# Kernel tuning notes

Hardware: AMD Instinct MI355X
Metric: run time of the kernel (lower is better)

Reference implementation:

```python
import jax, jax.numpy as jnp
import numpy as np

HEADS = 12
DIM_HEAD = 64
SCALE = DIM_HEAD ** -0.5


def setup_inputs() -> dict:
    key = jax.random.key(0)
    k1, k2, k3 = jax.random.split(key, 3)
    B, N, D = 4, 2048, 768
    inner = HEADS * DIM_HEAD  # 768
    x = jax.random.normal(k1, (B, N, D), dtype=jnp.float32)
    W_qkv = jax.random.normal(k2, (D, 3 * inner), dtype=jnp.float32) * (D ** -0.5)
    W_out = jax.random.normal(k3, (inner, D), dtype=jnp.float32) * (inner ** -0.5)
    b_out = jnp.zeros((D,), dtype=jnp.float32)
    return {"x": x, "W_qkv": W_qkv, "W_out": W_out, "b_out": b_out}


def reference(x, W_qkv, W_out, b_out):
    B, N, D = x.shape
    qkv = x @ W_qkv  # [B, N, 3*inner]
    q, k, v = jnp.split(qkv, 3, axis=-1)
    # 'b n (h d) -> b h n d'
    def split_heads(t):
        return t.reshape(B, N, HEADS, DIM_HEAD).transpose(0, 2, 1, 3)
    q, k, v = split_heads(q), split_heads(k), split_heads(v)
    dots = jnp.einsum('bhnd,bhmd->bhnm', q, k) * SCALE  # [B, H, N, N]
    attn = jax.nn.softmax(dots, axis=-1)
    out = jnp.einsum('bhnm,bhmd->bhnd', attn, v)
    out = out.transpose(0, 2, 1, 3).reshape(B, N, HEADS * DIM_HEAD)  # 'b h n d -> b n (h d)'
    return out @ W_out + b_out
```

## Files before the change

### kernel.cpp

```cpp
#include <hip/hip_runtime.h>
#include <hip/hip_bf16.h>

typedef __bf16 bf16_t;
typedef __bf16 bf16x4 __attribute__((ext_vector_type(4)));
typedef __bf16 bf16x8 __attribute__((ext_vector_type(8)));
typedef float f32x4 __attribute__((ext_vector_type(4)));

#define HEADS 12
#define DHEAD 64
#define NSEQ 2048
#define BATCH 4
#define DMODEL 768
#define NINNER 768

__device__ __forceinline__ void gl_lds16(const bf16_t* g, bf16_t* l) {
  __builtin_amdgcn_global_load_lds(
      (const __attribute__((address_space(1))) void*)g,
      (__attribute__((address_space(3))) void*)l, 16, 0, 0);
}

__device__ __forceinline__ int swz(int row, int colElem) {
  return row * 64 + (colElem ^ ((row & 7) << 3));
}

__global__ void cast_bf16_kernel(const float* __restrict__ in, bf16_t* __restrict__ out, int n8) {
  int i = blockIdx.x * blockDim.x + threadIdx.x;
  const int stride = gridDim.x * blockDim.x;
  for (; i < n8; i += stride) {
    const f32x4* p = (const f32x4*)(in + (size_t)i * 8);
    f32x4 a = p[0], b = p[1];
    bf16x8 o;
#pragma unroll
    for (int j = 0; j < 4; ++j) { o[j] = (bf16_t)a[j]; o[j + 4] = (bf16_t)b[j]; }
    *(bf16x8*)(out + (size_t)i * 8) = o;
  }
}

__global__ void transpose_cast_kernel(const float* __restrict__ in, bf16_t* __restrict__ out,
                                      int K, int N) {
  __shared__ float tile[32][33];
  const int bx = blockIdx.x * 32;
  const int by = blockIdx.y * 32;
  const int tx = threadIdx.x, ty = threadIdx.y;
#pragma unroll
  for (int i = ty; i < 32; i += 8)
    tile[i][tx] = in[(size_t)(by + i) * N + bx + tx];
  __syncthreads();
#pragma unroll
  for (int i = ty; i < 32; i += 8)
    out[(size_t)(bx + i) * K + by + tx] = (bf16_t)tile[tx][i];
}

template <int MODE>
__global__ __launch_bounds__(256, 2)
void gemm_bt(const bf16_t* __restrict__ A, const bf16_t* __restrict__ Bt,
             bf16_t* __restrict__ qw, bf16_t* __restrict__ kw, bf16_t* __restrict__ vtw,
             const float* __restrict__ bias, float* __restrict__ outf,
             int M, int Nn, int K) {
  __shared__ bf16_t As[128 * 64];
  __shared__ bf16_t Bs[128 * 64];
  const int tid = threadIdx.x;
  const int wid = tid >> 6;
  const int lane = tid & 63;
  const int m0 = blockIdx.x * 128;
  const int n0 = blockIdx.y * 128;
  const int arow = lane >> 3;
  const int acol = (lane & 7) * 8;
  const int wm = (wid >> 1) * 64;
  const int wn = (wid & 1) * 64;
  const int fr = lane & 15;
  const int fg = lane >> 4;

  f32x4 acc[4][4] = {};

  for (int kt = 0; kt < K; kt += 64) {
    __syncthreads();
#pragma unroll
    for (int i = 0; i < 4; ++i) {
      const int c = i * 4 + wid;
      gl_lds16(A + (size_t)(m0 + c * 8 + arow) * K + kt + acol, As + c * 512);
      gl_lds16(Bt + (size_t)(n0 + c * 8 + arow) * K + kt + acol, Bs + c * 512);
    }
    __syncthreads();
#pragma unroll
    for (int kk = 0; kk < 2; ++kk) {
      bf16x8 af[4], bfr[4];
#pragma unroll
      for (int mi = 0; mi < 4; ++mi)
        af[mi] = *(const bf16x8*)(As + (wm + mi * 16 + fr) * 64 + kk * 32 + fg * 8);
#pragma unroll
      for (int ni = 0; ni < 4; ++ni)
        bfr[ni] = *(const bf16x8*)(Bs + (wn + ni * 16 + fr) * 64 + kk * 32 + fg * 8);
#pragma unroll
      for (int mi = 0; mi < 4; ++mi)
#pragma unroll
        for (int ni = 0; ni < 4; ++ni)
          acc[mi][ni] = __builtin_amdgcn_mfma_f32_16x16x32_bf16(af[mi], bfr[ni], acc[mi][ni], 0, 0, 0);
    }
  }

  if (MODE == 0 && n0 >= 2 * NINNER) {
#pragma unroll
    for (int mi = 0; mi < 4; ++mi) {
#pragma unroll
      for (int ni = 0; ni < 4; ++ni) {
        const int col = n0 + wn + ni * 16 + fr - 2 * NINNER;
        const int h = col >> 6, d = col & 63;
        const int row0 = m0 + wm + mi * 16 + fg * 4;
        const int b = row0 >> 11, n = row0 & 2047;
        bf16x4 pk;
#pragma unroll
        for (int r = 0; r < 4; ++r) pk[r] = (bf16_t)acc[mi][ni][r];
        *(bf16x4*)(vtw + ((size_t)((b * HEADS + h) * DHEAD + d)) * NSEQ + n) = pk;
      }
    }
  } else {
#pragma unroll
    for (int mi = 0; mi < 4; ++mi) {
#pragma unroll
      for (int ni = 0; ni < 4; ++ni) {
#pragma unroll
        for (int r = 0; r < 4; ++r) {
          const int row = m0 + wm + mi * 16 + fg * 4 + r;
          const int col = n0 + wn + ni * 16 + fr;
          float val = acc[mi][ni][r];
          if (MODE == 0) {
            const int which = col / NINNER;
            const int cin = col - which * NINNER;
            const int h = cin >> 6, d = cin & 63;
            const int b = row >> 11, n = row & 2047;
            bf16_t* dst = (which == 0) ? qw : kw;
            if (which == 0) val *= 0.125f;
            dst[(((size_t)(b * HEADS + h)) * NSEQ + n) * DHEAD + d] = (bf16_t)val;
          } else {
            outf[(size_t)row * Nn + col] = val + bias[col];
          }
        }
      }
    }
  }
}

__global__ __launch_bounds__(256, 3)
void attn_fwd(const bf16_t* __restrict__ qg, const bf16_t* __restrict__ kg,
              const bf16_t* __restrict__ vtg, bf16_t* __restrict__ og) {
  __shared__ bf16_t Ks[2][64 * 64];
  __shared__ bf16_t Vs[2][64 * 64];
  __shared__ bf16_t Ps[4 * 32 * 64];
  const int tid = threadIdx.x, wid = tid >> 6, lane = tid & 63;
  const int logical = (blockIdx.x & 7) * 96 + (blockIdx.x >> 3);
  const int bh = logical >> 4;
  const int qbase = (logical & 15) * 128 + wid * 32;
  const bf16_t* Q = qg + (size_t)bh * NSEQ * DHEAD;
  const bf16_t* K = kg + (size_t)bh * NSEQ * DHEAD;
  const bf16_t* Vt = vtg + (size_t)bh * NSEQ * DHEAD;
  const int fr = lane & 15, fg = lane >> 4;

  bf16x8 qf[2][2];
#pragma unroll
  for (int mi = 0; mi < 2; ++mi)
#pragma unroll
    for (int ks = 0; ks < 2; ++ks)
      qf[mi][ks] = *(const bf16x8*)(Q + (size_t)(qbase + mi * 16 + fr) * DHEAD + ks * 32 + fg * 8);

  f32x4 oacc[2][4] = {};
  float lsum[2][4] = {{0.f, 0.f, 0.f, 0.f}, {0.f, 0.f, 0.f, 0.f}};
  bf16_t* myP = Ps + wid * (32 * 64);

  const int krow = lane >> 3;
  const int ksrc = ((lane & 7) ^ krow) << 3;

#pragma unroll
  for (int i = 0; i < 2; ++i) {
    const int c = wid * 2 + i;
    gl_lds16(K + (size_t)(c * 8 + krow) * DHEAD + ksrc, &Ks[0][c * 512]);
    gl_lds16(Vt + (size_t)(c * 8 + krow) * NSEQ + ksrc, &Vs[0][c * 512]);
  }

  for (int t = 0; t < NSEQ / 64; ++t) {
    const int buf = t & 1;
    __syncthreads();

    if (t + 1 < NSEQ / 64) {
      const int kv = (t + 1) * 64;
#pragma unroll
      for (int i = 0; i < 2; ++i) {
        const int c = wid * 2 + i;
        gl_lds16(K + (size_t)(kv + c * 8 + krow) * DHEAD + ksrc, &Ks[buf ^ 1][c * 512]);
        gl_lds16(Vt + (size_t)(c * 8 + krow) * NSEQ + kv + ksrc, &Vs[buf ^ 1][c * 512]);
      }
    }

    f32x4 sacc[2][4] = {};
    __builtin_amdgcn_s_setprio(1);
#pragma unroll
    for (int ks = 0; ks < 2; ++ks) {
      bf16x8 kf[4];
#pragma unroll
      for (int ni = 0; ni < 4; ++ni)
        kf[ni] = *(const bf16x8*)(&Ks[buf][swz(ni * 16 + fr, ks * 32 + fg * 8)]);
#pragma unroll
      for (int mi = 0; mi < 2; ++mi)
#pragma unroll
        for (int ni = 0; ni < 4; ++ni)
          sacc[mi][ni] = __builtin_amdgcn_mfma_f32_16x16x32_bf16(qf[mi][ks], kf[ni], sacc[mi][ni], 0, 0, 0);
    }
    __builtin_amdgcn_s_setprio(0);

#pragma unroll
    for (int mi = 0; mi < 2; ++mi) {
#pragma unroll
      for (int r = 0; r < 4; ++r) {
        float rs = 0.f;
#pragma unroll
        for (int ni = 0; ni < 4; ++ni) {
          float p = __expf(sacc[mi][ni][r]);
          sacc[mi][ni][r] = p;
          rs += p;
        }
        lsum[mi][r] += rs;
      }
    }

#pragma unroll
    for (int mi = 0; mi < 2; ++mi)
#pragma unroll
      for (int ni = 0; ni < 4; ++ni)
#pragma unroll
        for (int r = 0; r < 4; ++r) {
          const int row = mi * 16 + fg * 4 + r;
          myP[row * 64 + ((ni * 16 + fr) ^ ((row & 7) << 3))] = (bf16_t)sacc[mi][ni][r];
        }
    asm volatile("s_waitcnt lgkmcnt(0)" ::: "memory");
    __builtin_amdgcn_sched_barrier(0);

    __builtin_amdgcn_s_setprio(1);
#pragma unroll
    for (int ks = 0; ks < 2; ++ks) {
      bf16x8 pf[2], vf[4];
#pragma unroll
      for (int mi = 0; mi < 2; ++mi)
        pf[mi] = *(const bf16x8*)(myP + swz(mi * 16 + fr, ks * 32 + fg * 8));
#pragma unroll
      for (int di = 0; di < 4; ++di)
        vf[di] = *(const bf16x8*)(&Vs[buf][swz(di * 16 + fr, ks * 32 + fg * 8)]);
#pragma unroll
      for (int mi = 0; mi < 2; ++mi)
#pragma unroll
        for (int di = 0; di < 4; ++di)
          oacc[mi][di] = __builtin_amdgcn_mfma_f32_16x16x32_bf16(pf[mi], vf[di], oacc[mi][di], 0, 0, 0);
    }
    __builtin_amdgcn_s_setprio(0);
  }

#pragma unroll
  for (int mi = 0; mi < 2; ++mi)
#pragma unroll
    for (int r = 0; r < 4; ++r) {
      float rs = lsum[mi][r];
#pragma unroll
      for (int mk = 8; mk >= 1; mk >>= 1) rs += __shfl_xor(rs, mk, 64);
      lsum[mi][r] = rs;
    }

  const int b = bh / HEADS, h = bh % HEADS;
#pragma unroll
  for (int mi = 0; mi < 2; ++mi) {
#pragma unroll
    for (int r = 0; r < 4; ++r) {
      const int n = qbase + mi * 16 + fg * 4 + r;
      const float inv = 1.0f / lsum[mi][r];
#pragma unroll
      for (int di = 0; di < 4; ++di)
        og[((size_t)b * NSEQ + n) * DMODEL + h * DHEAD + di * 16 + fr] =
            (bf16_t)(oacc[mi][di][r] * inv);
    }
  }
}

extern "C" void kernel_launch(void* const* d_in, const int* in_sizes, int n_in,
                              void* d_out, int out_size, void* d_ws, size_t ws_size,
                              hipStream_t stream) {
  const float* x    = (const float*)d_in[0];
  const float* Wqkv = (const float*)d_in[1];
  const float* Wout = (const float*)d_in[2];
  const float* bout = (const float*)d_in[3];
  float* out = (float*)d_out;

  char* ws = (char*)d_ws;
  bf16_t* xb    = (bf16_t*)(ws + 0);
  bf16_t* wqkvT = (bf16_t*)(ws + 12582912);
  bf16_t* woutT = (bf16_t*)(ws + 16121856);
  bf16_t* qw    = (bf16_t*)(ws + 17301504);
  bf16_t* kw    = (bf16_t*)(ws + 29884416);
  bf16_t* vtw   = (bf16_t*)(ws + 42467328);
  bf16_t* attno = (bf16_t*)(ws + 55050240);

  cast_bf16_kernel<<<1024, 256, 0, stream>>>(x, xb, (8192 * 768) / 8);
  transpose_cast_kernel<<<dim3(2304 / 32, 768 / 32), dim3(32, 8), 0, stream>>>(Wqkv, wqkvT, 768, 2304);
  transpose_cast_kernel<<<dim3(768 / 32, 768 / 32), dim3(32, 8), 0, stream>>>(Wout, woutT, 768, 768);

  gemm_bt<0><<<dim3(64, 18), 256, 0, stream>>>(xb, wqkvT, qw, kw, vtw, nullptr, nullptr,
                                               8192, 2304, 768);
  attn_fwd<<<768, 256, 0, stream>>>(qw, kw, vtw, attno);
  gemm_bt<1><<<dim3(64, 6), 256, 0, stream>>>(attno, woutT, nullptr, nullptr, nullptr, bout, out,
                                              8192, 768, 768);
}
```

Baseline: 159.2 us.

## Rewrite attention core with 32x32 MFMA and register-resident P via lane shuffles

Switches the attention kernel from 16x16x32 to 32x32x16 bf16 MFMA tiles and computes S transposed (K as the A operand), so P stays in registers. P is packed to bf16 and exchanged across half-waves with shuffles instead of going through an LDS round-trip. K/V staging becomes a single unswizzled buffer laid out in per-fragment order, and the row-sum reduction shrinks to one cross-half shuffle. This removes the P LDS stores and loads, the lgkmcnt wait and the swizzle arithmetic, but adds shuffle traffic and more accumulator registers, which puts the 3-wave occupancy target at risk.

```diff
diff --git a/kernel.cpp b/kernel.cpp
--- a/kernel.cpp
+++ b/kernel.cpp
@@ -5,6 +5,8 @@
 typedef __bf16 bf16x4 __attribute__((ext_vector_type(4)));
 typedef __bf16 bf16x8 __attribute__((ext_vector_type(8)));
 typedef float f32x4 __attribute__((ext_vector_type(4)));
+typedef float f32x16 __attribute__((ext_vector_type(16)));
+typedef unsigned int u32x4 __attribute__((ext_vector_type(4)));
 
 #define HEADS 12
 #define DHEAD 64
@@ -19,8 +21,10 @@
       (__attribute__((address_space(3))) void*)l, 16, 0, 0);
 }
 
-__device__ __forceinline__ int swz(int row, int colElem) {
-  return row * 64 + (colElem ^ ((row & 7) << 3));
+__device__ __forceinline__ unsigned pack_bf16_2(float a, float b) {
+  unsigned lo = (unsigned)__builtin_bit_cast(unsigned short, (bf16_t)a);
+  unsigned hi = (unsigned)__builtin_bit_cast(unsigned short, (bf16_t)b);
+  return lo | (hi << 16);
 }
 
 __global__ void cast_bf16_kernel(const float* __restrict__ in, bf16_t* __restrict__ out, int n8) {
@@ -144,9 +148,7 @@
 __global__ __launch_bounds__(256, 3)
 void attn_fwd(const bf16_t* __restrict__ qg, const bf16_t* __restrict__ kg,
               const bf16_t* __restrict__ vtg, bf16_t* __restrict__ og) {
-  __shared__ bf16_t Ks[2][64 * 64];
-  __shared__ bf16_t Vs[2][64 * 64];
-  __shared__ bf16_t Ps[4 * 32 * 64];
+  __shared__ bf16_t KV[2][16 * 512];
   const int tid = threadIdx.x, wid = tid >> 6, lane = tid & 63;
   const int logical = (blockIdx.x & 7) * 96 + (blockIdx.x >> 3);
   const int bh = logical >> 4;
@@ -154,127 +156,102 @@
   const bf16_t* Q = qg + (size_t)bh * NSEQ * DHEAD;
   const bf16_t* K = kg + (size_t)bh * NSEQ * DHEAD;
   const bf16_t* Vt = vtg + (size_t)bh * NSEQ * DHEAD;
-  const int fr = lane & 15, fg = lane >> 4;
-
-  bf16x8 qf[2][2];
-#pragma unroll
-  for (int mi = 0; mi < 2; ++mi)
-#pragma unroll
-    for (int ks = 0; ks < 2; ++ks)
-      qf[mi][ks] = *(const bf16x8*)(Q + (size_t)(qbase + mi * 16 + fr) * DHEAD + ks * 32 + fg * 8);
-
-  f32x4 oacc[2][4] = {};
-  float lsum[2][4] = {{0.f, 0.f, 0.f, 0.f}, {0.f, 0.f, 0.f, 0.f}};
-  bf16_t* myP = Ps + wid * (32 * 64);
-
-  const int krow = lane >> 3;
-  const int ksrc = ((lane & 7) ^ krow) << 3;
-
-#pragma unroll
-  for (int i = 0; i < 2; ++i) {
-    const int c = wid * 2 + i;
-    gl_lds16(K + (size_t)(c * 8 + krow) * DHEAD + ksrc, &Ks[0][c * 512]);
-    gl_lds16(Vt + (size_t)(c * 8 + krow) * NSEQ + ksrc, &Vs[0][c * 512]);
-  }
+  const int l31 = lane & 31, hi = lane >> 5;
+
+  bf16x8 qf[4];
+#pragma unroll
+  for (int ks = 0; ks < 4; ++ks)
+    qf[ks] = *(const bf16x8*)(Q + (size_t)(qbase + l31) * DHEAD + ks * 16 + hi * 8);
+
+  f32x16 oacc[2] = {};
+  float lsum = 0.f;
+
+  auto stage = [&](int bsel, int t) {
+    const int kv0 = t * 64;
+#pragma unroll
+    for (int i = 0; i < 4; ++i) {
+      const int c = wid * 4 + i;
+      bf16_t* dst = &KV[bsel][c * 512];
+      if (c < 8) {
+        gl_lds16(K + (size_t)(kv0 + (c >> 2) * 32 + l31) * DHEAD + (c & 3) * 16 + hi * 8, dst);
+      } else {
+        gl_lds16(Vt + (size_t)(((c >> 2) & 1) * 32 + l31) * NSEQ + kv0 + (c & 3) * 16 + hi * 8, dst);
+      }
+    }
+  };
+
+  stage(0, 0);
 
   for (int t = 0; t < NSEQ / 64; ++t) {
     const int buf = t & 1;
     __syncthreads();
-
-    if (t + 1 < NSEQ / 64) {
-      const int kv = (t + 1) * 64;
-#pragma unroll
-      for (int i = 0; i < 2; ++i) {
-        const int c = wid * 2 + i;
-        gl_lds16(K + (size_t)(kv + c * 8 + krow) * DHEAD + ksrc, &Ks[buf ^ 1][c * 512]);
-        gl_lds16(Vt + (size_t)(c * 8 + krow) * NSEQ + kv + ksrc, &Vs[buf ^ 1][c * 512]);
-      }
-    }
-
-    f32x4 sacc[2][4] = {};
+    if (t + 1 < NSEQ / 64) stage(buf ^ 1, t + 1);
+
+    const bf16_t* base = &KV[buf][0];
+
+    f32x16 sacc[2] = {};
     __builtin_amdgcn_s_setprio(1);
 #pragma unroll
-    for (int ks = 0; ks < 2; ++ks) {
-      bf16x8 kf[4];
-#pragma unroll
-      for (int ni = 0; ni < 4; ++ni)
-        kf[ni] = *(const bf16x8*)(&Ks[buf][swz(ni * 16 + fr, ks * 32 + fg * 8)]);
-#pragma unroll
-      for (int mi = 0; mi < 2; ++mi)
-#pragma unroll
-        for (int ni = 0; ni < 4; ++ni)
-          sacc[mi][ni] = __builtin_amdgcn_mfma_f32_16x16x32_bf16(qf[mi][ks], kf[ni], sacc[mi][ni], 0, 0, 0);
-    }
+    for (int mi = 0; mi < 2; ++mi)
+#pragma unroll
+      for (int ks = 0; ks < 4; ++ks) {
+        bf16x8 kf = *(const bf16x8*)(base + (mi * 4 + ks) * 512 + lane * 8);
+        sacc[mi] = __builtin_amdgcn_mfma_f32_32x32x16_bf16(kf, qf[ks], sacc[mi], 0, 0, 0);
+      }
     __builtin_amdgcn_s_setprio(0);
 
+    bf16x8 pa[4];
 #pragma unroll
     for (int mi = 0; mi < 2; ++mi) {
-#pragma unroll
-      for (int r = 0; r < 4; ++r) {
-        float rs = 0.f;
-#pragma unroll
-        for (int ni = 0; ni < 4; ++ni) {
-          float p = __expf(sacc[mi][ni][r]);
-          sacc[mi][ni][r] = p;
-          rs += p;
-        }
-        lsum[mi][r] += rs;
-      }
-    }
-
-#pragma unroll
-    for (int mi = 0; mi < 2; ++mi)
-#pragma unroll
-      for (int ni = 0; ni < 4; ++ni)
-#pragma unroll
-        for (int r = 0; r < 4; ++r) {
-          const int row = mi * 16 + fg * 4 + r;
-          myP[row * 64 + ((ni * 16 + fr) ^ ((row & 7) << 3))] = (bf16_t)sacc[mi][ni][r];
-        }
-    asm volatile("s_waitcnt lgkmcnt(0)" ::: "memory");
-    __builtin_amdgcn_sched_barrier(0);
+      float p[16];
+      float rs = 0.f;
+#pragma unroll
+      for (int r = 0; r < 16; ++r) {
+        p[r] = __expf(sacc[mi][r]);
+        rs += p[r];
+      }
+      lsum += rs;
+      unsigned W[8];
+#pragma unroll
+      for (int j = 0; j < 8; ++j) W[j] = pack_bf16_2(p[2 * j], p[2 * j + 1]);
+#pragma unroll
+      for (int s = 0; s < 2; ++s) {
+        const unsigned sendA = hi ? W[4 * s] : W[4 * s + 2];
+        const unsigned sendB = hi ? W[4 * s + 1] : W[4 * s + 3];
+        const unsigned recvA = __shfl_xor(sendA, 32, 64);
+        const unsigned recvB = __shfl_xor(sendB, 32, 64);
+        u32x4 pw;
+        pw[0] = hi ? recvA : W[4 * s];
+        pw[1] = hi ? recvB : W[4 * s + 1];
+        pw[2] = hi ? W[4 * s + 2] : recvA;
+        pw[3] = hi ? W[4 * s + 3] : recvB;
+        pa[mi * 2 + s] = __builtin_bit_cast(bf16x8, pw);
+      }
+    }
 
     __builtin_amdgcn_s_setprio(1);
 #pragma unroll
-    for (int ks = 0; ks < 2; ++ks) {
-      bf16x8 pf[2], vf[4];
-#pragma unroll
-      for (int mi = 0; mi < 2; ++mi)
-        pf[mi] = *(const bf16x8*)(myP + swz(mi * 16 + fr, ks * 32 + fg * 8));
-#pragma unroll
-      for (int di = 0; di < 4; ++di)
-        vf[di] = *(const bf16x8*)(&Vs[buf][swz(di * 16 + fr, ks * 32 + fg * 8)]);
-#pragma unroll
-      for (int mi = 0; mi < 2; ++mi)
-#pragma unroll
-        for (int di = 0; di < 4; ++di)
-          oacc[mi][di] = __builtin_amdgcn_mfma_f32_16x16x32_bf16(pf[mi], vf[di], oacc[mi][di], 0, 0, 0);
-    }
+    for (int ni = 0; ni < 2; ++ni)
+#pragma unroll
+      for (int ks = 0; ks < 4; ++ks) {
+        bf16x8 vf = *(const bf16x8*)(base + (8 + ni * 4 + ks) * 512 + lane * 8);
+        oacc[ni] = __builtin_amdgcn_mfma_f32_32x32x16_bf16(pa[ks], vf, oacc[ni], 0, 0, 0);
+      }
     __builtin_amdgcn_s_setprio(0);
   }
 
-#pragma unroll
-  for (int mi = 0; mi < 2; ++mi)
-#pragma unroll
-    for (int r = 0; r < 4; ++r) {
-      float rs = lsum[mi][r];
-#pragma unroll
-      for (int mk = 8; mk >= 1; mk >>= 1) rs += __shfl_xor(rs, mk, 64);
-      lsum[mi][r] = rs;
-    }
-
+  lsum += __shfl_xor(lsum, 32, 64);
+  const float inv0 = 1.0f / lsum;
   const int b = bh / HEADS, h = bh % HEADS;
 #pragma unroll
-  for (int mi = 0; mi < 2; ++mi) {
-#pragma unroll
-    for (int r = 0; r < 4; ++r) {
-      const int n = qbase + mi * 16 + fg * 4 + r;
-      const float inv = 1.0f / lsum[mi][r];
-#pragma unroll
-      for (int di = 0; di < 4; ++di)
-        og[((size_t)b * NSEQ + n) * DMODEL + h * DHEAD + di * 16 + fr] =
-            (bf16_t)(oacc[mi][di][r] * inv);
-    }
+  for (int r = 0; r < 16; ++r) {
+    const int qq = (r & 3) + 8 * (r >> 2) + 4 * hi;
+    const float invr = __shfl(inv0, qq, 64);
+    const int n = qbase + qq;
+#pragma unroll
+    for (int ni = 0; ni < 2; ++ni)
+      og[((size_t)b * NSEQ + n) * DMODEL + h * DHEAD + ni * 32 + l31] =
+          (bf16_t)(oacc[ni][r] * invr);
   }
 }
 
```

After: 159.2 us. About the same (-0.0%).
